# Kernel optimization log

Hardware: AMD Instinct MI355X
Metric: run time of the kernel (lower is better)

The kernel has to match this reference:

```python
import jax, jax.numpy as jnp
import numpy as np

T, B, TD, HD, VD = 64, 4096, 512, 256, 484
LN_EPS = 1e-5   # torch nn.LayerNorm default
COS_EPS = 1e-8  # torch F.cosine_similarity default


def setup_inputs() -> dict:
    key = jax.random.key(0)
    ks = jax.random.split(key, 6)
    w = lambda k, shape: jax.random.normal(k, shape, dtype=jnp.float32) * 0.02
    return {
        "t_feat": jax.random.normal(ks[0], (B, TD), dtype=jnp.float32),
        "W1": w(ks[1], (T, HD, TD)),            # torch Linear weight layout [out, in]
        "b1": w(ks[2], (T, HD)),
        "gamma": jnp.ones((T, HD), jnp.float32),
        "beta": jnp.zeros((T, HD), jnp.float32),
        "W2": w(ks[3], (T, VD, HD)),
        "b2": w(ks[4], (T, VD)),
        "centroids": jax.random.normal(ks[5], (T, VD), dtype=jnp.float32),
    }


def reference(t_feat, W1, b1, gamma, beta, W2, b2, centroids):
    # All T per-task mappers batched into one grouped GEMM pipeline.
    # Linear1: [B, TD] x [T, HD, TD] -> [T, B, HD]
    h = jnp.einsum("bd,thd->tbh", t_feat, W1) + b1[:, None, :]
    # LayerNorm over hidden dim (per task affine params)
    mu = jnp.mean(h, axis=-1, keepdims=True)
    var = jnp.mean(jnp.square(h - mu), axis=-1, keepdims=True)
    h = (h - mu) * jax.lax.rsqrt(var + LN_EPS) * gamma[:, None, :] + beta[:, None, :]
    # Exact GELU (torch nn.GELU default uses erf)
    h = jax.nn.gelu(h, approximate=False)
    # Linear2: [T, B, HD] x [T, VD, HD] -> [T, B, VD] predicted visual features
    v = jnp.einsum("tbh,tvh->tbv", h, W2) + b2[:, None, :]
    # Cosine similarity vs each task centroid (eps-clamped norms, as in torch)
    v_norm = jnp.maximum(jnp.linalg.norm(v, axis=-1), COS_EPS)          # [T, B]
    c_norm = jnp.maximum(jnp.linalg.norm(centroids, axis=-1), COS_EPS)  # [T]
    cos = jnp.einsum("tbv,tv->tb", v, centroids) / (v_norm * c_norm[:, None])
    distances = jnp.mean(1.0 - cos, axis=-1)  # [T] mean cosine distance per task
    best_task = jnp.argmin(distances)          # top-1 routing decision
    return distances, best_task
```

## Files before the change

kernel.cpp:

```cpp
#include <hip/hip_runtime.h>
#include <math.h>

#define TASKS 64
#define NB    4096
#define TDI   512
#define HDI   256
#define VDI   484

#define WS_TF   ((size_t)0)
#define WS_W1   ((size_t)4194304)
#define WS_W2   ((size_t)20971520)
#define WS_CN   ((size_t)37748736)
#define WS_BC   ((size_t)37748992)
#define WS_ACC  ((size_t)37749248)
#define WS_WCP  ((size_t)37749504)

#define LDS_HP 0
#define LDS_B2 32768
#define LDS_R0 34816
#define LDS_R1 35840
#define LDS_MU 36864
#define LDS_RS 37120
#define SMEM_BYTES 37376

typedef _Float16 half8 __attribute__((ext_vector_type(8)));
typedef float    f32x4 __attribute__((ext_vector_type(4)));

#define MFMA16(a, b, c) __builtin_amdgcn_mfma_f32_16x16x32_f16((a), (b), (c), 0, 0, 0)

__device__ __forceinline__ float gelu_exact(float x) {
  float az = fabsf(x) * 0.70710678118654752f;
  float d  = fmaf(0.3275911f, az, 1.0f);
  float t; asm("v_rcp_f32 %0, %1" : "=v"(t) : "v"(d));
  float p  = fmaf(t, 1.061405429f, -1.453152027f);
  p = fmaf(t, p, 1.421413741f);
  p = fmaf(t, p, -0.284496736f);
  p = fmaf(t, p, 0.254829592f);
  p = p * t;
  float m = az * az * -1.4426950408889634f;
  float e; asm("v_exp_f32 %0, %1" : "=v"(e) : "v"(m));
  float er = fmaf(-p, e, 1.0f);
  er = copysignf(er, x);
  float hx = 0.5f * x;
  return fmaf(hx, er, hx);
}

extern "C" __global__ void __launch_bounds__(256, 8)
prep_all(const float* __restrict__ t_feat,
         const float* __restrict__ W1,
         const float* __restrict__ W2,
         const float* __restrict__ cent,
         _Float16* __restrict__ tf,
         _Float16* __restrict__ w1,
         _Float16* __restrict__ w2,
         float* __restrict__ wcp) {
  __shared__ __align__(16) char pbuf[17408];
  const int bid = blockIdx.x, tid = threadIdx.x;

  if (bid < 256) {
    int t = bid >> 2, q = bid & 3;
    int h = tid;
    int vs = q * 121;
    const float* wp = W2 + ((size_t)t * VDI + vs) * HDI + h;
    const float* cp = cent + (size_t)t * VDI + vs;
    float s = 0.f;
    int v = 0;
    #pragma unroll 1
    for (; v + 8 <= 121; v += 8) {
      float x0 = wp[0 * 256], x1 = wp[1 * 256], x2 = wp[2 * 256], x3 = wp[3 * 256];
      float x4 = wp[4 * 256], x5 = wp[5 * 256], x6 = wp[6 * 256], x7 = wp[7 * 256];
      s = fmaf(x0, cp[v + 0], s); s = fmaf(x1, cp[v + 1], s);
      s = fmaf(x2, cp[v + 2], s); s = fmaf(x3, cp[v + 3], s);
      s = fmaf(x4, cp[v + 4], s); s = fmaf(x5, cp[v + 5], s);
      s = fmaf(x6, cp[v + 6], s); s = fmaf(x7, cp[v + 7], s);
      wp += 8 * 256;
    }
    s = fmaf(wp[0], cp[v], s);
    wcp[((size_t)q * 64 + t) * 256 + h] = s;
    return;
  }

  const float* src;
  half8* dst;
  int w2vdBase = -1;

  if (bid < 512) {
    int g = bid - 256;
    int rb = g >> 2, kq = g & 3;
    src = t_feat + (size_t)rb * 64 * 512 + kq * 128;
    dst = (half8*)tf + ((size_t)rb * 4096 + kq * 1024);
  } else if (bid < 1536) {
    int g = bid - 512;
    int t = g >> 4, w_ = (g >> 2) & 3, kq = g & 3;
    src = W1 + ((size_t)t * 256 + w_ * 64) * 512 + kq * 128;
    dst = (half8*)w1 + ((size_t)t * 16384 + w_ * 4096 + kq * 1024);
  } else {
    int g = bid - 1536;
    int t = g >> 4, sub = g & 15;
    int p = sub >> 3, w_ = (sub >> 1) & 3, kq = sub & 1;
    src = W2 + (size_t)t * 484 * 256 + kq * 128;
    w2vdBase = p * 256 + w_ * 64;
    dst = (half8*)w2 + ((size_t)t * 16384 + p * 8192 + w_ * 2048 + kq * 1024);
  }

  const int srcStride = (w2vdBase < 0) ? 512 : 256;
  ushort* lds = (ushort*)pbuf;
  #pragma unroll
  for (int j = 0; j < 8; ++j) {
    int f = j * 256 + tid;
    int row = f >> 5, kc = f & 31;
    float4 v0 = make_float4(0.f, 0.f, 0.f, 0.f);
    if (w2vdBase < 0) {
      v0 = ((const float4*)(src + (size_t)row * srcStride))[kc];
    } else {
      int vd = w2vdBase + row;
      if (vd < VDI) v0 = ((const float4*)(src + (size_t)vd * 256))[kc];
    }
    _Float16 h4[4] = {(_Float16)v0.x, (_Float16)v0.y, (_Float16)v0.z, (_Float16)v0.w};
    *(ushort4*)(&lds[row * 136 + kc * 4]) = *(const ushort4*)h4;
  }
  __syncthreads();

  #pragma unroll
  for (int j = 0; j < 4; ++j) {
    int u = j * 256 + tid;
    int ksl = u >> 8, rg = (u >> 6) & 3, q = (u >> 4) & 3, l15 = u & 15;
    int row = rg * 16 + l15, k8l = ksl * 4 + q;
    dst[u] = *(const half8*)(pbuf + row * 272 + k8l * 16);
  }
}

extern "C" __global__ void prep_fin(const float* __restrict__ wcp,
                                    const float* __restrict__ b2,
                                    const float* __restrict__ cent,
                                    _Float16* __restrict__ w2,
                                    float* __restrict__ cnorm,
                                    float* __restrict__ bc,
                                    float* __restrict__ accum) {
  __shared__ float redc[256], redb[256];
  const int t = blockIdx.x, h = threadIdx.x;
  float wc = wcp[((size_t)0 * 64 + t) * 256 + h] + wcp[((size_t)1 * 64 + t) * 256 + h]
           + wcp[((size_t)2 * 64 + t) * 256 + h] + wcp[((size_t)3 * 64 + t) * 256 + h];
  int ks = h >> 5, q = (h >> 3) & 3;
  size_t o = (size_t)t * 16384 + 8192 + 3 * 2048 + ks * 256 + 2 * 64 + q * 16 + 4;
  w2[o * 8 + (h & 7)] = (_Float16)wc;

  float c2 = 0.f, b2c = 0.f;
  for (int v = h; v < VDI; v += 256) {
    float c = cent[(size_t)t * VDI + v];
    c2 += c * c;
    b2c += b2[(size_t)t * VDI + v] * c;
  }
  redc[h] = c2; redb[h] = b2c;
  __syncthreads();
  if (h < 64) {
    c2  = redc[h] + redc[h + 64] + redc[h + 128] + redc[h + 192];
    b2c = redb[h] + redb[h + 64] + redb[h + 128] + redb[h + 192];
    #pragma unroll
    for (int off = 32; off; off >>= 1) { c2 += __shfl_xor(c2, off); b2c += __shfl_xor(b2c, off); }
    if (h == 0) { cnorm[t] = sqrtf(c2); bc[t] = b2c; accum[t] = 0.f; }
  }
}


#define STEP_RELOAD(A, ACC, PB) do {                                           \
  __builtin_amdgcn_s_setprio(1);                                               \
  _Pragma("unroll") for (int ct_ = 0; ct_ < 4; ++ct_) {                        \
    ACC[0][ct_] = MFMA16(A[0], b[ct_], ACC[0][ct_]);                           \
    ACC[1][ct_] = MFMA16(A[1], b[ct_], ACC[1][ct_]);                           \
    ACC[2][ct_] = MFMA16(A[2], b[ct_], ACC[2][ct_]);                           \
    ACC[3][ct_] = MFMA16(A[3], b[ct_], ACC[3][ct_]);                           \
    b[ct_] = (PB)[ct_ * 64];                                                   \
  }                                                                            \
  __builtin_amdgcn_s_setprio(0);                                               \
} while (0)

#define STEP_LAST(A, ACC) do {                                                 \
  __builtin_amdgcn_s_setprio(1);                                               \
  _Pragma("unroll") for (int ct_ = 0; ct_ < 4; ++ct_) {                        \
    ACC[0][ct_] = MFMA16(A[0], b[ct_], ACC[0][ct_]);                           \
    ACC[1][ct_] = MFMA16(A[1], b[ct_], ACC[1][ct_]);                           \
    ACC[2][ct_] = MFMA16(A[2], b[ct_], ACC[2][ct_]);                           \
    ACC[3][ct_] = MFMA16(A[3], b[ct_], ACC[3][ct_]);                           \
  }                                                                            \
  __builtin_amdgcn_s_setprio(0);                                               \
} while (0)

#define LD_A4(D, P) do { D[0] = (P)[0]; D[1] = (P)[64]; D[2] = (P)[128]; D[3] = (P)[192]; } while (0)

#define P3_STEP(ACC, HN) do {                                                  \
  __builtin_amdgcn_s_setprio(1);                                               \
  ACC[0][0]=MFMA16(a0[0],b[0],ACC[0][0]); ACC[1][0]=MFMA16(a0[1],b[0],ACC[1][0]); \
  ACC[2][0]=MFMA16(a0[2],b[0],ACC[2][0]); ACC[3][0]=MFMA16(a0[3],b[0],ACC[3][0]); \
  b[0]=pc[0];                                                                  \
  ACC[0][1]=MFMA16(a0[0],b[1],ACC[0][1]); ACC[1][1]=MFMA16(a0[1],b[1],ACC[1][1]); \
  ACC[2][1]=MFMA16(a0[2],b[1],ACC[2][1]); ACC[3][1]=MFMA16(a0[3],b[1],ACC[3][1]); \
  b[1]=pc[64];                                                                 \
  ACC[0][2]=MFMA16(a0[0],b[2],ACC[0][2]); ACC[1][2]=MFMA16(a0[1],b[2],ACC[1][2]); \
  ACC[2][2]=MFMA16(a0[2],b[2],ACC[2][2]); ACC[3][2]=MFMA16(a0[3],b[2],ACC[3][2]); \
  b[2]=pc[128];                                                                \
  ACC[0][3]=MFMA16(a0[0],b[3],ACC[0][3]); a0[0]=*(const half8*)(HN);           \
  ACC[1][3]=MFMA16(a0[1],b[3],ACC[1][3]); a0[1]=*(const half8*)((HN)+1024);    \
  ACC[2][3]=MFMA16(a0[2],b[3],ACC[2][3]); a0[2]=*(const half8*)((HN)+2048);    \
  ACC[3][3]=MFMA16(a0[3],b[3],ACC[3][3]); a0[3]=*(const half8*)((HN)+3072);    \
  b[3]=pc[192]; pc+=256;                                                       \
  __builtin_amdgcn_s_setprio(0);                                               \
} while (0)

extern "C" __global__ void __launch_bounds__(256, 4)
router_main(const half8* __restrict__ tfv,
            const half8* __restrict__ w1v,
            const half8* __restrict__ w2v,
            const float* __restrict__ b1,
            const float* __restrict__ gamma,
            const float* __restrict__ beta,
            const float* __restrict__ b2,
            const float* __restrict__ bc,
            const float* __restrict__ cnorm,
            float* __restrict__ accum) {
  __shared__ __align__(16) char smem[SMEM_BYTES];

  const int tid = threadIdx.x;
  const int bx  = blockIdx.x;
  const int t  = ((bx & 7) << 3) | (bx >> 9);
  const int rb = (bx >> 3) & 63;

  const int lane = tid & 63;
  const int w    = tid >> 6;
  const int quad = lane >> 4;
  const int l15  = lane & 15;

  f32x4 zero4 = {0.f, 0.f, 0.f, 0.f};
  f32x4 acc[4][4];
  #pragma unroll
  for (int rt = 0; rt < 4; ++rt)
    #pragma unroll
    for (int ct = 0; ct < 4; ++ct) acc[rt][ct] = zero4;

  half8 a0[4], a1[4], b[4];

  {
    const half8* pa = tfv + ((size_t)rb * 4096 + quad * 16 + l15);
    const half8* pb = w1v + ((size_t)t * 16384 + w * 4096 + quad * 16 + l15);
    LD_A4(a0, pa);
    b[0] = pb[0]; b[1] = pb[64]; b[2] = pb[128]; b[3] = pb[192];
    a1[0] = pa[256]; a1[1] = pa[320]; a1[2] = pa[384]; a1[3] = pa[448];
    pa += 512;
    pb += 256;
    #pragma unroll 1
    for (int ks = 0; ks < 14; ks += 2) {
      STEP_RELOAD(a0, acc, pb); pb += 256;
      LD_A4(a0, pa);            pa += 256;
      STEP_RELOAD(a1, acc, pb); pb += 256;
      LD_A4(a1, pa);            pa += 256;
    }
    STEP_RELOAD(a0, acc, pb);
    STEP_LAST(a1, acc);
  }

  float b1v[4];
  #pragma unroll
  for (int ct = 0; ct < 4; ++ct)
    b1v[ct] = b1[t * HDI + w * 64 + ct * 16 + l15];
  {
    float* red0 = (float*)(smem + LDS_R0);
    float* red1 = (float*)(smem + LDS_R1);
    #pragma unroll
    for (int rt = 0; rt < 4; ++rt)
      #pragma unroll
      for (int r = 0; r < 4; ++r) {
        float sv = 0.f, qv = 0.f;
        #pragma unroll
        for (int ct = 0; ct < 4; ++ct) {
          float v = acc[rt][ct][r] + b1v[ct];
          acc[rt][ct][r] = v;
          sv += v; qv += v * v;
        }
        sv += __shfl_xor(sv, 1); qv += __shfl_xor(qv, 1);
        sv += __shfl_xor(sv, 2); qv += __shfl_xor(qv, 2);
        sv += __shfl_xor(sv, 4); qv += __shfl_xor(qv, 4);
        sv += __shfl_xor(sv, 8); qv += __shfl_xor(qv, 8);
        if (l15 == 0) {
          int m = rt * 16 + quad * 4 + r;
          red0[w * 64 + m] = sv;
          red1[w * 64 + m] = qv;
        }
      }
    __syncthreads();
    if (tid < 64) {
      float s = red0[tid] + red0[64 + tid] + red0[128 + tid] + red0[192 + tid];
      float q = red1[tid] + red1[64 + tid] + red1[128 + tid] + red1[192 + tid];
      float mu = s * (1.f / HDI);
      float var = q * (1.f / HDI) - mu * mu;
      ((float*)(smem + LDS_MU))[tid] = mu;
      ((float*)(smem + LDS_RS))[tid] = rsqrtf(var + 1e-5f);
    }
    float gvv[4], bevv[4];
    #pragma unroll
    for (int ct = 0; ct < 4; ++ct) {
      gvv[ct]  = gamma[t * HDI + w * 64 + ct * 16 + l15];
      bevv[ct] = beta [t * HDI + w * 64 + ct * 16 + l15];
    }
    {
      float* b2s = (float*)(smem + LDS_B2);
      int i0 = tid;
      b2s[i0] = (i0 < VDI) ? b2[(size_t)t * VDI + i0] : 0.f;
      int i1 = tid + 256;
      float v = 0.f;
      if (i1 < VDI) v = b2[(size_t)t * VDI + i1];
      else if (i1 == VDI) v = bc[t];
      b2s[i1] = v;
    }
    __syncthreads();
    const float* mus = (const float*)(smem + LDS_MU);
    const float* rss = (const float*)(smem + LDS_RS);
    #pragma unroll
    for (int rt = 0; rt < 4; ++rt) {
      float m4[4], s4[4];
      #pragma unroll
      for (int r = 0; r < 4; ++r) {
        int m = rt * 16 + quad * 4 + r;
        m4[r] = mus[m]; s4[r] = rss[m];
      }
      #pragma unroll
      for (int ct = 0; ct < 4; ++ct) {
        int col = w * 64 + ct * 16 + l15;
        int base = (((col >> 5) * 4 + rt) * 4 + ((col >> 3) & 3)) * 256
                 + quad * 64 + (l15 & 7) * 2;
        #pragma unroll
        for (int r = 0; r < 4; ++r) {
          float x = (acc[rt][ct][r] - m4[r]) * s4[r];
          x = x * gvv[ct] + bevv[ct];
          *(_Float16*)(smem + LDS_HP + base + r * 16) = (_Float16)gelu_exact(x);
        }
      }
    }
    __syncthreads();
  }

  {
    const float* b2s = (const float*)(smem + LDS_B2);
    float* red0 = (float*)(smem + LDS_R0);
    float* red1 = (float*)(smem + LDS_R1);
    const char* ha = smem + LDS_HP + quad * 256 + l15 * 16;

    #pragma unroll 1
    for (int pass = 0; pass < 2; ++pass) {
      const half8* pc = w2v + ((size_t)t * 16384 + pass * 8192 + w * 2048 + quad * 16 + l15);
      f32x4 acc2[4][4];
      #pragma unroll
      for (int rt = 0; rt < 4; ++rt)
        #pragma unroll
        for (int ct = 0; ct < 4; ++ct) acc2[rt][ct] = zero4;

      a0[0] = *(const half8*)(ha);        a0[1] = *(const half8*)(ha + 1024);
      a0[2] = *(const half8*)(ha + 2048); a0[3] = *(const half8*)(ha + 3072);
      b[0] = pc[0]; b[1] = pc[64]; b[2] = pc[128]; b[3] = pc[192];
      pc += 256;
      #pragma unroll 1
      for (int ks = 0; ks < 7; ++ks) {
        P3_STEP(acc2, ha + (ks + 1) * 4096);
      }
      STEP_LAST(a0, acc2);

      #pragma unroll
      for (int rt = 0; rt < 4; ++rt)
        #pragma unroll
        for (int r = 0; r < 4; ++r) {
          float ssq = 0.f, dtv = 0.f;
          #pragma unroll
          for (int ct = 0; ct < 4; ++ct) {
            int vcol = pass * 256 + w * 64 + ct * 16 + l15;
            float val = acc2[rt][ct][r] + b2s[vcol];
            ssq += (vcol < VDI) ? val * val : 0.f;
            dtv += (vcol == VDI) ? val : 0.f;
          }
          ssq += __shfl_xor(ssq, 1); dtv += __shfl_xor(dtv, 1);
          ssq += __shfl_xor(ssq, 2); dtv += __shfl_xor(dtv, 2);
          ssq += __shfl_xor(ssq, 4); dtv += __shfl_xor(dtv, 4);
          ssq += __shfl_xor(ssq, 8); dtv += __shfl_xor(dtv, 8);
          if (l15 == 0) {
            int m = rt * 16 + quad * 4 + r;
            if (pass == 0) {
              red0[w * 64 + m] = ssq;
            } else {
              red0[w * 64 + m] += ssq;
              red1[w * 64 + m] = dtv;
            }
          }
        }
    }

    __syncthreads();
    if (tid < 64) {
      float ss  = red0[tid] + red0[64 + tid] + red0[128 + tid] + red0[192 + tid];
      float dot = red1[tid] + red1[64 + tid] + red1[128 + tid] + red1[192 + tid];
      float cn = fmaxf(cnorm[t], 1e-8f);
      float vn = fmaxf(sqrtf(ss), 1e-8f);
      float part = 1.0f - dot / (vn * cn);
      part += __shfl_down(part, 32);
      part += __shfl_down(part, 16);
      part += __shfl_down(part, 8);
      part += __shfl_down(part, 4);
      part += __shfl_down(part, 2);
      part += __shfl_down(part, 1);
      if (tid == 0) atomicAdd(accum + t, part);
    }
  }
}

extern "C" __global__ void finalize_k(const float* __restrict__ accum, float* __restrict__ out) {
  int t = threadIdx.x;
  float d = accum[t] * (1.0f / (float)NB);
  out[t] = d;
  float bd = d; int bi = t;
  #pragma unroll
  for (int off = 32; off; off >>= 1) {
    float od = __shfl_xor(bd, off);
    int   oi = __shfl_xor(bi, off);
    if (od < bd || (od == bd && oi < bi)) { bd = od; bi = oi; }
  }
  if (t == 0) out[64] = (float)bi;
}

extern "C" void kernel_launch(void* const* d_in, const int* in_sizes, int n_in,
                              void* d_out, int out_size, void* d_ws, size_t ws_size,
                              hipStream_t stream) {
  const float* t_feat = (const float*)d_in[0];
  const float* W1     = (const float*)d_in[1];
  const float* b1     = (const float*)d_in[2];
  const float* gamma  = (const float*)d_in[3];
  const float* beta   = (const float*)d_in[4];
  const float* W2     = (const float*)d_in[5];
  const float* b2     = (const float*)d_in[6];
  const float* cent   = (const float*)d_in[7];

  char* ws = (char*)d_ws;
  _Float16* tf = (_Float16*)(ws + WS_TF);
  _Float16* w1 = (_Float16*)(ws + WS_W1);
  _Float16* w2 = (_Float16*)(ws + WS_W2);
  float* cnorm = (float*)(ws + WS_CN);
  float* bc    = (float*)(ws + WS_BC);
  float* accum = (float*)(ws + WS_ACC);
  float* wcp   = (float*)(ws + WS_WCP);
  float* out = (float*)d_out;

  prep_all<<<2560, 256, 0, stream>>>(t_feat, W1, W2, cent, tf, w1, w2, wcp);
  prep_fin<<<64, 256, 0, stream>>>(wcp, b2, cent, w2, cnorm, bc, accum);
  router_main<<<4096, 256, 0, stream>>>((const half8*)tf, (const half8*)w1, (const half8*)w2,
                                        b1, gamma, beta, b2, bc, cnorm, accum);
  finalize_k<<<1, 64, 0, stream>>>(accum, out);
}
```

Measured before the change: 317.7 us.

## Stage GEMM1 A tiles via global_load_lds double buffering instead of direct global loads

Result: no change. 316.0 us (-0.5%).

```diff
diff --git a/kernel.cpp b/kernel.cpp
--- a/kernel.cpp
+++ b/kernel.cpp
@@ -27,6 +27,11 @@
 typedef float    f32x4 __attribute__((ext_vector_type(4)));
 
 #define MFMA16(a, b, c) __builtin_amdgcn_mfma_f32_16x16x32_f16((a), (b), (c), 0, 0, 0)
+
+__device__ __forceinline__ void gld_lds16(const void* g, void* l) {
+  __builtin_amdgcn_global_load_lds((const __attribute__((address_space(1))) void*)g,
+                                   (__attribute__((address_space(3))) void*)l, 16, 0, 0);
+}
 
 __device__ __forceinline__ float gelu_exact(float x) {
   float az = fabsf(x) * 0.70710678118654752f;
@@ -163,48 +168,60 @@
 }
 
 
-#define STEP_RELOAD(A, ACC, PB) do {                                           \
-  __builtin_amdgcn_s_setprio(1);                                               \
-  _Pragma("unroll") for (int ct_ = 0; ct_ < 4; ++ct_) {                        \
-    ACC[0][ct_] = MFMA16(A[0], b[ct_], ACC[0][ct_]);                           \
-    ACC[1][ct_] = MFMA16(A[1], b[ct_], ACC[1][ct_]);                           \
-    ACC[2][ct_] = MFMA16(A[2], b[ct_], ACC[2][ct_]);                           \
-    ACC[3][ct_] = MFMA16(A[3], b[ct_], ACC[3][ct_]);                           \
-    b[ct_] = (PB)[ct_ * 64];                                                   \
-  }                                                                            \
-  __builtin_amdgcn_s_setprio(0);                                               \
-} while (0)
-
-#define STEP_LAST(A, ACC) do {                                                 \
-  __builtin_amdgcn_s_setprio(1);                                               \
-  _Pragma("unroll") for (int ct_ = 0; ct_ < 4; ++ct_) {                        \
-    ACC[0][ct_] = MFMA16(A[0], b[ct_], ACC[0][ct_]);                           \
-    ACC[1][ct_] = MFMA16(A[1], b[ct_], ACC[1][ct_]);                           \
-    ACC[2][ct_] = MFMA16(A[2], b[ct_], ACC[2][ct_]);                           \
-    ACC[3][ct_] = MFMA16(A[3], b[ct_], ACC[3][ct_]);                           \
-  }                                                                            \
-  __builtin_amdgcn_s_setprio(0);                                               \
-} while (0)
-
-#define LD_A4(D, P) do { D[0] = (P)[0]; D[1] = (P)[64]; D[2] = (P)[128]; D[3] = (P)[192]; } while (0)
-
-#define P3_STEP(ACC, HN) do {                                                  \
+#define STEP_AB(ACC, PBP, HN) do {                                             \
   __builtin_amdgcn_s_setprio(1);                                               \
   ACC[0][0]=MFMA16(a0[0],b[0],ACC[0][0]); ACC[1][0]=MFMA16(a0[1],b[0],ACC[1][0]); \
   ACC[2][0]=MFMA16(a0[2],b[0],ACC[2][0]); ACC[3][0]=MFMA16(a0[3],b[0],ACC[3][0]); \
-  b[0]=pc[0];                                                                  \
+  b[0]=(PBP)[0];                                                               \
   ACC[0][1]=MFMA16(a0[0],b[1],ACC[0][1]); ACC[1][1]=MFMA16(a0[1],b[1],ACC[1][1]); \
   ACC[2][1]=MFMA16(a0[2],b[1],ACC[2][1]); ACC[3][1]=MFMA16(a0[3],b[1],ACC[3][1]); \
-  b[1]=pc[64];                                                                 \
+  b[1]=(PBP)[64];                                                              \
   ACC[0][2]=MFMA16(a0[0],b[2],ACC[0][2]); ACC[1][2]=MFMA16(a0[1],b[2],ACC[1][2]); \
   ACC[2][2]=MFMA16(a0[2],b[2],ACC[2][2]); ACC[3][2]=MFMA16(a0[3],b[2],ACC[3][2]); \
-  b[2]=pc[128];                                                                \
+  b[2]=(PBP)[128];                                                             \
   ACC[0][3]=MFMA16(a0[0],b[3],ACC[0][3]); a0[0]=*(const half8*)(HN);           \
   ACC[1][3]=MFMA16(a0[1],b[3],ACC[1][3]); a0[1]=*(const half8*)((HN)+1024);    \
   ACC[2][3]=MFMA16(a0[2],b[3],ACC[2][3]); a0[2]=*(const half8*)((HN)+2048);    \
   ACC[3][3]=MFMA16(a0[3],b[3],ACC[3][3]); a0[3]=*(const half8*)((HN)+3072);    \
-  b[3]=pc[192]; pc+=256;                                                       \
+  b[3]=(PBP)[192]; (PBP)+=256;                                                 \
   __builtin_amdgcn_s_setprio(0);                                               \
+} while (0)
+
+#define STEP_BO(ACC, PBP) do {                                                 \
+  __builtin_amdgcn_s_setprio(1);                                               \
+  _Pragma("unroll") for (int ct_ = 0; ct_ < 4; ++ct_) {                        \
+    ACC[0][ct_] = MFMA16(a0[0], b[ct_], ACC[0][ct_]);                          \
+    ACC[1][ct_] = MFMA16(a0[1], b[ct_], ACC[1][ct_]);                          \
+    ACC[2][ct_] = MFMA16(a0[2], b[ct_], ACC[2][ct_]);                          \
+    ACC[3][ct_] = MFMA16(a0[3], b[ct_], ACC[3][ct_]);                          \
+    b[ct_] = (PBP)[ct_ * 64];                                                  \
+  }                                                                            \
+  (PBP) += 256;                                                                \
+  __builtin_amdgcn_s_setprio(0);                                               \
+} while (0)
+
+#define STEP_LAST(ACC) do {                                                    \
+  __builtin_amdgcn_s_setprio(1);                                               \
+  _Pragma("unroll") for (int ct_ = 0; ct_ < 4; ++ct_) {                        \
+    ACC[0][ct_] = MFMA16(a0[0], b[ct_], ACC[0][ct_]);                          \
+    ACC[1][ct_] = MFMA16(a0[1], b[ct_], ACC[1][ct_]);                          \
+    ACC[2][ct_] = MFMA16(a0[2], b[ct_], ACC[2][ct_]);                          \
+    ACC[3][ct_] = MFMA16(a0[3], b[ct_], ACC[3][ct_]);                          \
+  }                                                                            \
+  __builtin_amdgcn_s_setprio(0);                                               \
+} while (0)
+
+#define LD_A4L(D, P) do {                                                      \
+  D[0] = *(const half8*)(P);        D[1] = *(const half8*)((P) + 1024);        \
+  D[2] = *(const half8*)((P) + 2048); D[3] = *(const half8*)((P) + 3072); } while (0)
+
+#define STAGE_A(Q, BUF) do {                                                   \
+  const half8* gs_ = gA + (Q) * 1024 + tid;                                    \
+  char* lb_ = (BUF) + (size_t)w * 1024;                                        \
+  gld_lds16(gs_,       lb_);                                                   \
+  gld_lds16(gs_ + 256, lb_ + 4096);                                            \
+  gld_lds16(gs_ + 512, lb_ + 8192);                                            \
+  gld_lds16(gs_ + 768, lb_ + 12288);                                           \
 } while (0)
 
 extern "C" __global__ void __launch_bounds__(256, 4)
@@ -237,25 +254,46 @@
     #pragma unroll
     for (int ct = 0; ct < 4; ++ct) acc[rt][ct] = zero4;
 
-  half8 a0[4], a1[4], b[4];
+  half8 a0[4], b[4];
 
   {
-    const half8* pa = tfv + ((size_t)rb * 4096 + quad * 16 + l15);
+    const half8* gA = tfv + (size_t)rb * 4096;
+    char* buf0 = smem + LDS_HP;
+    char* buf1 = smem + LDS_HP + 16384;
     const half8* pb = w1v + ((size_t)t * 16384 + w * 4096 + quad * 16 + l15);
-    LD_A4(a0, pa);
-    b[0] = pb[0]; b[1] = pb[64]; b[2] = pb[128]; b[3] = pb[192];
-    a1[0] = pa[256]; a1[1] = pa[320]; a1[2] = pa[384]; a1[3] = pa[448];
-    pa += 512;
-    pb += 256;
-    #pragma unroll 1
-    for (int ks = 0; ks < 14; ks += 2) {
-      STEP_RELOAD(a0, acc, pb); pb += 256;
-      LD_A4(a0, pa);            pa += 256;
-      STEP_RELOAD(a1, acc, pb); pb += 256;
-      LD_A4(a1, pa);            pa += 256;
-    }
-    STEP_RELOAD(a0, acc, pb);
-    STEP_LAST(a1, acc);
+    const char* hav0 = buf0 + quad * 256 + l15 * 16;
+    const char* hav1 = buf1 + quad * 256 + l15 * 16;
+
+    STAGE_A(0, buf0);
+    STAGE_A(1, buf1);
+    b[0] = pb[0]; b[1] = pb[64]; b[2] = pb[128]; b[3] = pb[192]; pb += 256;
+    __syncthreads();
+
+    LD_A4L(a0, hav0);
+    STEP_AB(acc, pb, hav0 + 4096);
+    STEP_AB(acc, pb, hav0 + 8192);
+    STEP_AB(acc, pb, hav0 + 12288);
+    STEP_BO(acc, pb);
+    __syncthreads();
+    STAGE_A(2, buf0);
+    LD_A4L(a0, hav1);
+    STEP_AB(acc, pb, hav1 + 4096);
+    STEP_AB(acc, pb, hav1 + 8192);
+    STEP_AB(acc, pb, hav1 + 12288);
+    STEP_BO(acc, pb);
+    __syncthreads();
+    STAGE_A(3, buf1);
+    LD_A4L(a0, hav0);
+    STEP_AB(acc, pb, hav0 + 4096);
+    STEP_AB(acc, pb, hav0 + 8192);
+    STEP_AB(acc, pb, hav0 + 12288);
+    STEP_BO(acc, pb);
+    __syncthreads();
+    LD_A4L(a0, hav1);
+    STEP_AB(acc, pb, hav1 + 4096);
+    STEP_AB(acc, pb, hav1 + 8192);
+    STEP_AB(acc, pb, hav1 + 12288);
+    STEP_LAST(acc);
   }
 
   float b1v[4];
@@ -353,15 +391,14 @@
         #pragma unroll
         for (int ct = 0; ct < 4; ++ct) acc2[rt][ct] = zero4;
 
-      a0[0] = *(const half8*)(ha);        a0[1] = *(const half8*)(ha + 1024);
-      a0[2] = *(const half8*)(ha + 2048); a0[3] = *(const half8*)(ha + 3072);
+      LD_A4L(a0, ha);
       b[0] = pc[0]; b[1] = pc[64]; b[2] = pc[128]; b[3] = pc[192];
       pc += 256;
       #pragma unroll 1
       for (int ks = 0; ks < 7; ++ks) {
-        P3_STEP(acc2, ha + (ks + 1) * 4096);
+        STEP_AB(acc2, pc, ha + (ks + 1) * 4096);
       }
-      STEP_LAST(a0, acc2);
+      STEP_LAST(acc2);
 
       #pragma unroll
       for (int rt = 0; rt < 4; ++rt)
```
